# Performance work log

Hardware: AMD Instinct MI355X
Metric: run time of the kernel (lower is better)

The kernel has to match this reference:

```python
import jax, jax.numpy as jnp
import numpy as np

IS_CAUSAL = True
NEG_INF = float('-inf')


def setup_inputs() -> dict:
    key = jax.random.key(0)
    kq, kk, kv = jax.random.split(key, 3)
    B, H, S, D = 4, 16, 2048, 64
    return {
        'query': jax.random.normal(kq, (B, H, S, D), dtype=jnp.float32),
        'key': jax.random.normal(kk, (B, H, S, D), dtype=jnp.float32),
        'value': jax.random.normal(kv, (B, H, S, D), dtype=jnp.float32),
    }


def reference(query, key, value):
    # Attention(Q,K,V) = softmax(QK^T / sqrt(d_k) + causal_mask) V
    d_k = query.shape[-1]
    scale = 1.0 / np.sqrt(d_k).astype(np.float32)
    # [B,H,Sq,Sk]
    scores = jnp.einsum('bhqd,bhkd->bhqk', query, key) * scale
    if IS_CAUSAL:
        sq, sk = query.shape[-2], key.shape[-2]
        causal = jnp.triu(jnp.ones((sq, sk), dtype=bool), k=1)
        scores = jnp.where(causal[None, None, :, :], NEG_INF, scores)
    weights = jax.nn.softmax(scores, axis=-1)
    # dropout p=0.0 (eval): identity
    out = jnp.einsum('bhqk,bhkd->bhqd', weights, value)
    return out
```

## Files before the change

### kernel.cpp

```cpp
#include <hip/hip_runtime.h>
#include <stdint.h>


#define SLEN 2048
#define DHEAD 64
#define NHEADS 64
#define NELEM (SLEN * DHEAD * NHEADS)
#define PADP 72

typedef short bf16x8 __attribute__((ext_vector_type(8)));
typedef float f32x4 __attribute__((ext_vector_type(4)));

__device__ __forceinline__ uint32_t pkbf(float hi, float lo) {
    uint32_t a = __builtin_bit_cast(uint32_t, lo) + 0x8000u;
    uint32_t b = __builtin_bit_cast(uint32_t, hi) + 0x8000u;
    return __builtin_amdgcn_perm(b, a, 0x07060302u);
}
__device__ __forceinline__ unsigned short f2bf(float f) {
    return (unsigned short)((__builtin_bit_cast(uint32_t, f) + 0x8000u) >> 16);
}
__device__ __forceinline__ int swz(int row, int g) {
    return row * 64 + ((g ^ (row & 7)) << 3);
}

__global__ __launch_bounds__(256)
void convert_prep(const float* __restrict__ K, const float* __restrict__ V,
                  unsigned short* __restrict__ Kb, unsigned short* __restrict__ Vtb) {
    __shared__ unsigned short Lt[64 * 264];
    const int b = blockIdx.x, t = threadIdx.x;
    if (b < 4096) {
        const int off = (b * 256 + t) * 8;
        float4 a = *(const float4*)(K + off);
        float4 c = *(const float4*)(K + off + 4);
        uint4 o;
        o.x = pkbf(a.y, a.x); o.y = pkbf(a.w, a.z);
        o.z = pkbf(c.y, c.x); o.w = pkbf(c.w, c.z);
        *(uint4*)(Kb + off) = o;
    } else {
        const int vb2 = b - 4096;
        const int head = vb2 >> 3, kblk = vb2 & 7;
        const float* Vh = V + (size_t)head * (SLEN * DHEAD) + kblk * 256 * DHEAD;
        unsigned short* Vo = Vtb + (size_t)head * (SLEN * DHEAD) + kblk * 256;
#pragma unroll
        for (int i = 0; i < 16; ++i) {
            int idx = t + 256 * i;
            int key = idx >> 4, d4 = idx & 15;
            float4 v = *(const float4*)(Vh + key * DHEAD + d4 * 4);
            Lt[(d4 * 4 + 0) * 264 + key] = f2bf(v.x);
            Lt[(d4 * 4 + 1) * 264 + key] = f2bf(v.y);
            Lt[(d4 * 4 + 2) * 264 + key] = f2bf(v.z);
            Lt[(d4 * 4 + 3) * 264 + key] = f2bf(v.w);
        }
        __syncthreads();
#pragma unroll
        for (int j = 0; j < 8; ++j) {
            int idx = t + 256 * j;
            int d = idx >> 5, k8 = idx & 31;
            *(uint4*)(Vo + (size_t)d * SLEN + k8 * 8) = *(const uint4*)(Lt + d * 264 + k8 * 8);
        }
    }
}

__global__ __launch_bounds__(512, 4)
void sdpa_mfma(const float* __restrict__ Qf, const unsigned short* __restrict__ Kb,
               const unsigned short* __restrict__ Vtb, float* __restrict__ Og) {
    const int n    = blockIdx.x;
    const int half = n >> 8, idx = n & 255;
    const int head = idx >> 2, r4 = idx & 3;
    const int qb   = (half == 0) ? (4 + r4) : (3 - r4);
    const int q0   = qb * 256;

    const size_t hb = (size_t)head * SLEN * DHEAD;
    const float* Qh = Qf + hb;
    const unsigned short* Kh  = Kb + hb;
    const unsigned short* Vth = Vtb + hb;
    float* Oh = Og + hb;

    const int tid  = threadIdx.x;
    const int w    = tid >> 6, lane = tid & 63;
    const int cl   = lane & 15, quad = lane >> 4;

    __shared__ unsigned short Kl[64 * 64];
    __shared__ unsigned short Vt[64 * 64];
    __shared__ unsigned short Pl[8 * 32 * PADP];

    const int qw = q0 + w * 32;
    unsigned short* Plw = Pl + w * 32 * PADP;

    bf16x8 qf[2][2];
#pragma unroll
    for (int m = 0; m < 2; ++m)
#pragma unroll
        for (int h = 0; h < 2; ++h) {
            const float* src = Qh + (size_t)(qw + m * 16 + cl) * DHEAD + h * 32 + quad * 8;
            float4 a = *(const float4*)src;
            float4 c = *(const float4*)(src + 4);
            uint4 u;
            u.x = pkbf(a.y, a.x); u.y = pkbf(a.w, a.z);
            u.z = pkbf(c.y, c.x); u.w = pkbf(c.w, c.z);
            qf[m][h] = __builtin_bit_cast(bf16x8, u);
        }

    f32x4 o[2][4];
#pragma unroll
    for (int m = 0; m < 2; ++m)
#pragma unroll
        for (int d = 0; d < 4; ++d) o[m][d] = (f32x4){0.f, 0.f, 0.f, 0.f};
    float ls[2] = {0.f, 0.f};
    const float SCL = 0.18033688f;

    const int srow = tid >> 3, sg = tid & 7;
    const int ldsOff = swz(srow, sg);
    const size_t kSrc = (size_t)srow * DHEAD + sg * 8;
    const size_t vSrc = (size_t)srow * SLEN + sg * 8;

    const int ntiles = (qb + 1) * 4;
    uint4 kreg = *(const uint4*)(Kh + kSrc);
    uint4 vreg = *(const uint4*)(Vth + vSrc);

    for (int t = 0; t < ntiles; ++t) {
        const int k0 = t * 64;
        __syncthreads();
        *(uint4*)(Kl + ldsOff) = kreg;
        *(uint4*)(Vt + ldsOff) = vreg;
        __syncthreads();
        if (t + 1 < ntiles) {
            kreg = *(const uint4*)(Kh + kSrc + (size_t)(k0 + 64) * DHEAD);
            vreg = *(const uint4*)(Vth + vSrc + (k0 + 64));
        }
        if (k0 > qw + 31) continue;
        const bool partial = (k0 + 63 > qw);

        bf16x8 kb[4][2];
#pragma unroll
        for (int kk = 0; kk < 4; ++kk)
#pragma unroll
            for (int h = 0; h < 2; ++h)
                kb[kk][h] = __builtin_bit_cast(bf16x8,
                    *(const uint4*)(Kl + swz(kk * 16 + cl, h * 4 + quad)));

#pragma unroll
        for (int qq = 0; qq < 2; ++qq) {
            const int qrel = qw - k0 + qq * 16 + cl;
#pragma unroll
            for (int kk = 0; kk < 4; ++kk) {
                f32x4 s = (f32x4){0.f, 0.f, 0.f, 0.f};
                s = __builtin_amdgcn_mfma_f32_16x16x32_bf16(kb[kk][0], qf[qq][0], s, 0, 0, 0);
                s = __builtin_amdgcn_mfma_f32_16x16x32_bf16(kb[kk][1], qf[qq][1], s, 0, 0, 0);
                const int krel = kk * 16 + quad * 4;
                float p0, p1, p2, p3;
                if (partial) {
                    p0 = (krel + 0 <= qrel) ? __builtin_amdgcn_exp2f(s[0] * SCL) : 0.f;
                    p1 = (krel + 1 <= qrel) ? __builtin_amdgcn_exp2f(s[1] * SCL) : 0.f;
                    p2 = (krel + 2 <= qrel) ? __builtin_amdgcn_exp2f(s[2] * SCL) : 0.f;
                    p3 = (krel + 3 <= qrel) ? __builtin_amdgcn_exp2f(s[3] * SCL) : 0.f;
                } else {
                    p0 = __builtin_amdgcn_exp2f(s[0] * SCL);
                    p1 = __builtin_amdgcn_exp2f(s[1] * SCL);
                    p2 = __builtin_amdgcn_exp2f(s[2] * SCL);
                    p3 = __builtin_amdgcn_exp2f(s[3] * SCL);
                }
                ls[qq] += (p0 + p1) + (p2 + p3);
                uint2 pw;
                pw.x = pkbf(p1, p0);
                pw.y = pkbf(p3, p2);
                *(uint2*)(Plw + (qq * 16 + cl) * PADP + kk * 16 + quad * 4) = pw;
            }
        }

        bf16x8 pa[2][2], vbf[4][2];
#pragma unroll
        for (int m = 0; m < 2; ++m)
#pragma unroll
            for (int h = 0; h < 2; ++h)
                pa[m][h] = __builtin_bit_cast(bf16x8,
                    *(const uint4*)(Plw + (m * 16 + cl) * PADP + h * 32 + quad * 8));
#pragma unroll
        for (int dd = 0; dd < 4; ++dd)
#pragma unroll
            for (int h = 0; h < 2; ++h)
                vbf[dd][h] = __builtin_bit_cast(bf16x8,
                    *(const uint4*)(Vt + swz(dd * 16 + cl, h * 4 + quad)));

#pragma unroll
        for (int m = 0; m < 2; ++m)
#pragma unroll
            for (int dd = 0; dd < 4; ++dd) {
                o[m][dd] = __builtin_amdgcn_mfma_f32_16x16x32_bf16(pa[m][0], vbf[dd][0], o[m][dd], 0, 0, 0);
                o[m][dd] = __builtin_amdgcn_mfma_f32_16x16x32_bf16(pa[m][1], vbf[dd][1], o[m][dd], 0, 0, 0);
            }
    }

#pragma unroll
    for (int qq = 0; qq < 2; ++qq) {
        float v = ls[qq];
        v += __shfl_xor(v, 16);
        v += __shfl_xor(v, 32);
        ls[qq] = v;
    }

#pragma unroll
    for (int m = 0; m < 2; ++m)
#pragma unroll
        for (int r = 0; r < 4; ++r) {
            const float inv = 1.0f / __shfl(ls[m], quad * 4 + r);
#pragma unroll
            for (int dd = 0; dd < 4; ++dd)
                Oh[(size_t)(qw + m * 16 + quad * 4 + r) * DHEAD + dd * 16 + cl] = o[m][dd][r] * inv;
        }
}

extern "C" void kernel_launch(void* const* d_in, const int* in_sizes, int n_in,
                              void* d_out, int out_size, void* d_ws, size_t ws_size,
                              hipStream_t stream) {
    const float* Q = (const float*)d_in[0];
    const float* K = (const float*)d_in[1];
    const float* V = (const float*)d_in[2];
    float*       O = (float*)d_out;

    unsigned short* Kbf  = (unsigned short*)d_ws;
    unsigned short* Vtbf = Kbf + NELEM;

    convert_prep<<<dim3(4096 + 512), dim3(256), 0, stream>>>(K, V, Kbf, Vtbf);
    sdpa_mfma<<<dim3(512), dim3(512), 0, stream>>>(Q, Kbf, Vtbf, O);
}
```

Measured before the change: 219.5 us.

## Pair complementary 64-row query blocks per workgroup and shrink blocks to 256 threads

Each workgroup now has 4 waves covering two 64-row query blocks, A and 31-A. Their causal tile counts sum to a constant, so work per workgroup is balanced, and the grid doubles to 1024 blocks. Each thread loads two K/V vectors per tile. The K and V fragment loads are also interleaved with the MFMAs to cut register pressure. The cost is that waves owning block A sit idle during the later tiles that only block 31-A needs, while staying through the barriers.

```diff
diff --git a/kernel.cpp b/kernel.cpp
--- a/kernel.cpp
+++ b/kernel.cpp
@@ -53,22 +53,22 @@
         }
         __syncthreads();
 #pragma unroll
-        for (int j = 0; j < 8; ++j) {
-            int idx = t + 256 * j;
+        for (int jj = 0; jj < 8; ++jj) {
+            int idx = t + 256 * jj;
             int d = idx >> 5, k8 = idx & 31;
             *(uint4*)(Vo + (size_t)d * SLEN + k8 * 8) = *(const uint4*)(Lt + d * 264 + k8 * 8);
         }
     }
 }
 
-__global__ __launch_bounds__(512, 4)
+__global__ __launch_bounds__(256, 4)
 void sdpa_mfma(const float* __restrict__ Qf, const unsigned short* __restrict__ Kb,
                const unsigned short* __restrict__ Vtb, float* __restrict__ Og) {
-    const int n    = blockIdx.x;
-    const int half = n >> 8, idx = n & 255;
-    const int head = idx >> 2, r4 = idx & 3;
-    const int qb   = (half == 0) ? (4 + r4) : (3 - r4);
-    const int q0   = qb * 256;
+    const int n = blockIdx.x;
+    const int j = n >> 8, c = n & 255;
+    const int head = c & 63;
+    const int A  = (c >> 6) + 4 * j;
+    const int Bq = 31 - A;
 
     const size_t hb = (size_t)head * SLEN * DHEAD;
     const float* Qh = Qf + hb;
@@ -82,9 +82,9 @@
 
     __shared__ unsigned short Kl[64 * 64];
     __shared__ unsigned short Vt[64 * 64];
-    __shared__ unsigned short Pl[8 * 32 * PADP];
-
-    const int qw = q0 + w * 32;
+    __shared__ unsigned short Pl[4 * 32 * PADP];
+
+    const int qw = ((w < 2) ? A * 64 : Bq * 64) + (w & 1) * 32;
     unsigned short* Plw = Pl + w * 32 * PADP;
 
     bf16x8 qf[2][2];
@@ -94,10 +94,10 @@
         for (int h = 0; h < 2; ++h) {
             const float* src = Qh + (size_t)(qw + m * 16 + cl) * DHEAD + h * 32 + quad * 8;
             float4 a = *(const float4*)src;
-            float4 c = *(const float4*)(src + 4);
+            float4 b = *(const float4*)(src + 4);
             uint4 u;
             u.x = pkbf(a.y, a.x); u.y = pkbf(a.w, a.z);
-            u.z = pkbf(c.y, c.x); u.w = pkbf(c.w, c.z);
+            u.z = pkbf(b.y, b.x); u.w = pkbf(b.w, b.z);
             qf[m][h] = __builtin_bit_cast(bf16x8, u);
         }
 
@@ -109,66 +109,65 @@
     float ls[2] = {0.f, 0.f};
     const float SCL = 0.18033688f;
 
-    const int srow = tid >> 3, sg = tid & 7;
-    const int ldsOff = swz(srow, sg);
-    const size_t kSrc = (size_t)srow * DHEAD + sg * 8;
-    const size_t vSrc = (size_t)srow * SLEN + sg * 8;
-
-    const int ntiles = (qb + 1) * 4;
-    uint4 kreg = *(const uint4*)(Kh + kSrc);
-    uint4 vreg = *(const uint4*)(Vth + vSrc);
+    const int p1 = tid + 256;
+    const int srow0 = tid >> 3, sg0 = tid & 7;
+    const int srow1 = p1 >> 3,  sg1 = p1 & 7;
+    const int lo0 = swz(srow0, sg0), lo1 = swz(srow1, sg1);
+    const size_t kS0 = (size_t)srow0 * DHEAD + sg0 * 8, kS1 = (size_t)srow1 * DHEAD + sg1 * 8;
+    const size_t vS0 = (size_t)srow0 * SLEN + sg0 * 8,  vS1 = (size_t)srow1 * SLEN + sg1 * 8;
+
+    const int ntiles = Bq + 1;
+    uint4 kr0 = *(const uint4*)(Kh + kS0), kr1 = *(const uint4*)(Kh + kS1);
+    uint4 vr0 = *(const uint4*)(Vth + vS0), vr1 = *(const uint4*)(Vth + vS1);
 
     for (int t = 0; t < ntiles; ++t) {
         const int k0 = t * 64;
         __syncthreads();
-        *(uint4*)(Kl + ldsOff) = kreg;
-        *(uint4*)(Vt + ldsOff) = vreg;
+        *(uint4*)(Kl + lo0) = kr0; *(uint4*)(Kl + lo1) = kr1;
+        *(uint4*)(Vt + lo0) = vr0; *(uint4*)(Vt + lo1) = vr1;
         __syncthreads();
         if (t + 1 < ntiles) {
-            kreg = *(const uint4*)(Kh + kSrc + (size_t)(k0 + 64) * DHEAD);
-            vreg = *(const uint4*)(Vth + vSrc + (k0 + 64));
+            const size_t ko = (size_t)(k0 + 64) * DHEAD;
+            kr0 = *(const uint4*)(Kh + kS0 + ko);
+            kr1 = *(const uint4*)(Kh + kS1 + ko);
+            vr0 = *(const uint4*)(Vth + vS0 + (k0 + 64));
+            vr1 = *(const uint4*)(Vth + vS1 + (k0 + 64));
         }
         if (k0 > qw + 31) continue;
         const bool partial = (k0 + 63 > qw);
 
-        bf16x8 kb[4][2];
-#pragma unroll
-        for (int kk = 0; kk < 4; ++kk)
-#pragma unroll
-            for (int h = 0; h < 2; ++h)
-                kb[kk][h] = __builtin_bit_cast(bf16x8,
-                    *(const uint4*)(Kl + swz(kk * 16 + cl, h * 4 + quad)));
-
-#pragma unroll
-        for (int qq = 0; qq < 2; ++qq) {
-            const int qrel = qw - k0 + qq * 16 + cl;
-#pragma unroll
-            for (int kk = 0; kk < 4; ++kk) {
+#pragma unroll
+        for (int kk = 0; kk < 4; ++kk) {
+            bf16x8 kb0 = __builtin_bit_cast(bf16x8, *(const uint4*)(Kl + swz(kk * 16 + cl, quad)));
+            bf16x8 kb1 = __builtin_bit_cast(bf16x8, *(const uint4*)(Kl + swz(kk * 16 + cl, 4 + quad)));
+            const int krel = kk * 16 + quad * 4;
+#pragma unroll
+            for (int qq = 0; qq < 2; ++qq) {
                 f32x4 s = (f32x4){0.f, 0.f, 0.f, 0.f};
-                s = __builtin_amdgcn_mfma_f32_16x16x32_bf16(kb[kk][0], qf[qq][0], s, 0, 0, 0);
-                s = __builtin_amdgcn_mfma_f32_16x16x32_bf16(kb[kk][1], qf[qq][1], s, 0, 0, 0);
-                const int krel = kk * 16 + quad * 4;
-                float p0, p1, p2, p3;
+                s = __builtin_amdgcn_mfma_f32_16x16x32_bf16(kb0, qf[qq][0], s, 0, 0, 0);
+                s = __builtin_amdgcn_mfma_f32_16x16x32_bf16(kb1, qf[qq][1], s, 0, 0, 0);
+                float p0, p1v, p2, p3;
                 if (partial) {
+                    const int qrel = qw - k0 + qq * 16 + cl;
                     p0 = (krel + 0 <= qrel) ? __builtin_amdgcn_exp2f(s[0] * SCL) : 0.f;
-                    p1 = (krel + 1 <= qrel) ? __builtin_amdgcn_exp2f(s[1] * SCL) : 0.f;
+                    p1v = (krel + 1 <= qrel) ? __builtin_amdgcn_exp2f(s[1] * SCL) : 0.f;
                     p2 = (krel + 2 <= qrel) ? __builtin_amdgcn_exp2f(s[2] * SCL) : 0.f;
                     p3 = (krel + 3 <= qrel) ? __builtin_amdgcn_exp2f(s[3] * SCL) : 0.f;
                 } else {
                     p0 = __builtin_amdgcn_exp2f(s[0] * SCL);
-                    p1 = __builtin_amdgcn_exp2f(s[1] * SCL);
+                    p1v = __builtin_amdgcn_exp2f(s[1] * SCL);
                     p2 = __builtin_amdgcn_exp2f(s[2] * SCL);
                     p3 = __builtin_amdgcn_exp2f(s[3] * SCL);
                 }
-                ls[qq] += (p0 + p1) + (p2 + p3);
+                ls[qq] += (p0 + p1v) + (p2 + p3);
                 uint2 pw;
-                pw.x = pkbf(p1, p0);
+                pw.x = pkbf(p1v, p0);
                 pw.y = pkbf(p3, p2);
                 *(uint2*)(Plw + (qq * 16 + cl) * PADP + kk * 16 + quad * 4) = pw;
             }
         }
 
-        bf16x8 pa[2][2], vbf[4][2];
+        bf16x8 pa[2][2];
 #pragma unroll
         for (int m = 0; m < 2; ++m)
 #pragma unroll
@@ -176,19 +175,15 @@
                 pa[m][h] = __builtin_bit_cast(bf16x8,
                     *(const uint4*)(Plw + (m * 16 + cl) * PADP + h * 32 + quad * 8));
 #pragma unroll
-        for (int dd = 0; dd < 4; ++dd)
-#pragma unroll
-            for (int h = 0; h < 2; ++h)
-                vbf[dd][h] = __builtin_bit_cast(bf16x8,
-                    *(const uint4*)(Vt + swz(dd * 16 + cl, h * 4 + quad)));
-
-#pragma unroll
-        for (int m = 0; m < 2; ++m)
-#pragma unroll
-            for (int dd = 0; dd < 4; ++dd) {
-                o[m][dd] = __builtin_amdgcn_mfma_f32_16x16x32_bf16(pa[m][0], vbf[dd][0], o[m][dd], 0, 0, 0);
-                o[m][dd] = __builtin_amdgcn_mfma_f32_16x16x32_bf16(pa[m][1], vbf[dd][1], o[m][dd], 0, 0, 0);
+        for (int dd = 0; dd < 4; ++dd) {
+            bf16x8 vb0 = __builtin_bit_cast(bf16x8, *(const uint4*)(Vt + swz(dd * 16 + cl, quad)));
+            bf16x8 vb1 = __builtin_bit_cast(bf16x8, *(const uint4*)(Vt + swz(dd * 16 + cl, 4 + quad)));
+#pragma unroll
+            for (int m = 0; m < 2; ++m) {
+                o[m][dd] = __builtin_amdgcn_mfma_f32_16x16x32_bf16(pa[m][0], vb0, o[m][dd], 0, 0, 0);
+                o[m][dd] = __builtin_amdgcn_mfma_f32_16x16x32_bf16(pa[m][1], vb1, o[m][dd], 0, 0, 0);
             }
+        }
     }
 
 #pragma unroll
@@ -222,5 +217,5 @@
     unsigned short* Vtbf = Kbf + NELEM;
 
     convert_prep<<<dim3(4096 + 512), dim3(256), 0, stream>>>(K, V, Kbf, Vtbf);
-    sdpa_mfma<<<dim3(512), dim3(512), 0, stream>>>(Q, Kbf, Vtbf, O);
-}
+    sdpa_mfma<<<dim3(1024), dim3(256), 0, stream>>>(Q, Kbf, Vtbf, O);
+}
```

Measured after the change: 196.5 us. 1.12x faster.

## Rebalance causal attention into paired 64-row tiles with split-K across two waves

Applied to the files above, without the earlier changes.

Replaces the 512-thread blocks that stage K/V tiles in shared memory with 128-thread blocks (two waves). Each block handles a short query tile A and its mirrored long tile 31-A, splitting the long tile's key range between the waves and merging partial outputs and row sums through LDS. K and V fragments are now loaded straight from global/L2 with one-step register prefetch of K, and the softmax scale is folded into Q. This aims to balance causal work per block and drop the per-tile block-wide barriers, at the cost of redundant global reads of K/V per wave and far fewer threads per block.

```diff
diff --git a/kernel.cpp b/kernel.cpp
--- a/kernel.cpp
+++ b/kernel.cpp
@@ -7,6 +7,7 @@
 #define NHEADS 64
 #define NELEM (SLEN * DHEAD * NHEADS)
 #define PADP 72
+#define OMPAD 68
 
 typedef short bf16x8 __attribute__((ext_vector_type(8)));
 typedef float f32x4 __attribute__((ext_vector_type(4)));
@@ -18,9 +19,6 @@
 }
 __device__ __forceinline__ unsigned short f2bf(float f) {
     return (unsigned short)((__builtin_bit_cast(uint32_t, f) + 0x8000u) >> 16);
-}
-__device__ __forceinline__ int swz(int row, int g) {
-    return row * 64 + ((g ^ (row & 7)) << 3);
 }
 
 __global__ __launch_bounds__(256)
@@ -53,22 +51,21 @@
         }
         __syncthreads();
 #pragma unroll
-        for (int j = 0; j < 8; ++j) {
-            int idx = t + 256 * j;
+        for (int jj = 0; jj < 8; ++jj) {
+            int idx = t + 256 * jj;
             int d = idx >> 5, k8 = idx & 31;
             *(uint4*)(Vo + (size_t)d * SLEN + k8 * 8) = *(const uint4*)(Lt + d * 264 + k8 * 8);
         }
     }
 }
 
-__global__ __launch_bounds__(512, 4)
+__global__ __launch_bounds__(128, 2)
 void sdpa_mfma(const float* __restrict__ Qf, const unsigned short* __restrict__ Kb,
                const unsigned short* __restrict__ Vtb, float* __restrict__ Og) {
     const int n    = blockIdx.x;
-    const int half = n >> 8, idx = n & 255;
-    const int head = idx >> 2, r4 = idx & 3;
-    const int qb   = (half == 0) ? (4 + r4) : (3 - r4);
-    const int q0   = qb * 256;
+    const int head = n & 63;
+    const int A    = n >> 6;
+    const int TB   = 31 - A;
 
     const size_t hb = (size_t)head * SLEN * DHEAD;
     const float* Qh = Qf + hb;
@@ -80,134 +77,172 @@
     const int w    = tid >> 6, lane = tid & 63;
     const int cl   = lane & 15, quad = lane >> 4;
 
-    __shared__ unsigned short Kl[64 * 64];
-    __shared__ unsigned short Vt[64 * 64];
-    __shared__ unsigned short Pl[8 * 32 * PADP];
-
-    const int qw = q0 + w * 32;
-    unsigned short* Plw = Pl + w * 32 * PADP;
-
-    bf16x8 qf[2][2];
-#pragma unroll
-    for (int m = 0; m < 2; ++m)
-#pragma unroll
-        for (int h = 0; h < 2; ++h) {
-            const float* src = Qh + (size_t)(qw + m * 16 + cl) * DHEAD + h * 32 + quad * 8;
-            float4 a = *(const float4*)src;
-            float4 c = *(const float4*)(src + 4);
-            uint4 u;
-            u.x = pkbf(a.y, a.x); u.y = pkbf(a.w, a.z);
-            u.z = pkbf(c.y, c.x); u.w = pkbf(c.w, c.z);
-            qf[m][h] = __builtin_bit_cast(bf16x8, u);
-        }
-
-    f32x4 o[2][4];
-#pragma unroll
-    for (int m = 0; m < 2; ++m)
-#pragma unroll
-        for (int d = 0; d < 4; ++d) o[m][d] = (f32x4){0.f, 0.f, 0.f, 0.f};
-    float ls[2] = {0.f, 0.f};
+    __shared__ unsigned short Pl[2 * 64 * PADP];
+    __shared__ float Om[64 * OMPAD];
+    __shared__ float Lsm[64];
+
+    unsigned short* Plw = Pl + w * 64 * PADP;
     const float SCL = 0.18033688f;
 
-    const int srow = tid >> 3, sg = tid & 7;
-    const int ldsOff = swz(srow, sg);
-    const size_t kSrc = (size_t)srow * DHEAD + sg * 8;
-    const size_t vSrc = (size_t)srow * SLEN + sg * 8;
-
-    const int ntiles = (qb + 1) * 4;
-    uint4 kreg = *(const uint4*)(Kh + kSrc);
-    uint4 vreg = *(const uint4*)(Vth + vSrc);
-
-    for (int t = 0; t < ntiles; ++t) {
-        const int k0 = t * 64;
-        __syncthreads();
-        *(uint4*)(Kl + ldsOff) = kreg;
-        *(uint4*)(Vt + ldsOff) = vreg;
-        __syncthreads();
-        if (t + 1 < ntiles) {
-            kreg = *(const uint4*)(Kh + kSrc + (size_t)(k0 + 64) * DHEAD);
-            vreg = *(const uint4*)(Vth + vSrc + (k0 + 64));
-        }
-        if (k0 > qw + 31) continue;
-        const bool partial = (k0 + 63 > qw);
-
-        bf16x8 kb[4][2];
+    bf16x8 qf[4][2];
+    bf16x8 kbn[4][2];
+    f32x4  o[4][4];
+    float  ls[4];
+
+    auto load_qf = [&](int qw) {
+#pragma unroll
+        for (int m = 0; m < 4; ++m)
+#pragma unroll
+            for (int h = 0; h < 2; ++h) {
+                const float* src = Qh + (size_t)(qw + m * 16 + cl) * DHEAD + h * 32 + quad * 8;
+                float4 a = *(const float4*)src;
+                float4 b = *(const float4*)(src + 4);
+                uint4 u;
+                u.x = pkbf(a.y * SCL, a.x * SCL); u.y = pkbf(a.w * SCL, a.z * SCL);
+                u.z = pkbf(b.y * SCL, b.x * SCL); u.w = pkbf(b.w * SCL, b.z * SCL);
+                qf[m][h] = __builtin_bit_cast(bf16x8, u);
+            }
+    };
+    auto zero_acc = [&]() {
+#pragma unroll
+        for (int m = 0; m < 4; ++m) {
+            ls[m] = 0.f;
+#pragma unroll
+            for (int d = 0; d < 4; ++d) o[m][d] = (f32x4){0.f, 0.f, 0.f, 0.f};
+        }
+    };
+    auto load_kb = [&](int j, bf16x8 kb[4][2]) {
+        const unsigned short* base = Kh + (size_t)j * 64 * DHEAD;
 #pragma unroll
         for (int kk = 0; kk < 4; ++kk)
 #pragma unroll
             for (int h = 0; h < 2; ++h)
                 kb[kk][h] = __builtin_bit_cast(bf16x8,
-                    *(const uint4*)(Kl + swz(kk * 16 + cl, h * 4 + quad)));
-
-#pragma unroll
-        for (int qq = 0; qq < 2; ++qq) {
-            const int qrel = qw - k0 + qq * 16 + cl;
+                    *(const uint4*)(base + (kk * 16 + cl) * DHEAD + h * 32 + quad * 8));
+    };
+
+    auto do_steps = [&](int tq, int js, int je) {
+        if (js >= je) return;
+        load_kb(js, kbn);
+        for (int j = js; j < je; ++j) {
+            bf16x8 vb[4][2];
+            const unsigned short* vbase = Vth + j * 64;
+#pragma unroll
+            for (int dd = 0; dd < 4; ++dd)
+#pragma unroll
+                for (int h = 0; h < 2; ++h)
+                    vb[dd][h] = __builtin_bit_cast(bf16x8,
+                        *(const uint4*)(vbase + (size_t)(dd * 16 + cl) * SLEN + h * 32 + quad * 8));
+
+            const bool partial = (j == tq);
 #pragma unroll
             for (int kk = 0; kk < 4; ++kk) {
-                f32x4 s = (f32x4){0.f, 0.f, 0.f, 0.f};
-                s = __builtin_amdgcn_mfma_f32_16x16x32_bf16(kb[kk][0], qf[qq][0], s, 0, 0, 0);
-                s = __builtin_amdgcn_mfma_f32_16x16x32_bf16(kb[kk][1], qf[qq][1], s, 0, 0, 0);
                 const int krel = kk * 16 + quad * 4;
-                float p0, p1, p2, p3;
-                if (partial) {
-                    p0 = (krel + 0 <= qrel) ? __builtin_amdgcn_exp2f(s[0] * SCL) : 0.f;
-                    p1 = (krel + 1 <= qrel) ? __builtin_amdgcn_exp2f(s[1] * SCL) : 0.f;
-                    p2 = (krel + 2 <= qrel) ? __builtin_amdgcn_exp2f(s[2] * SCL) : 0.f;
-                    p3 = (krel + 3 <= qrel) ? __builtin_amdgcn_exp2f(s[3] * SCL) : 0.f;
-                } else {
-                    p0 = __builtin_amdgcn_exp2f(s[0] * SCL);
-                    p1 = __builtin_amdgcn_exp2f(s[1] * SCL);
-                    p2 = __builtin_amdgcn_exp2f(s[2] * SCL);
-                    p3 = __builtin_amdgcn_exp2f(s[3] * SCL);
+#pragma unroll
+                for (int qq = 0; qq < 4; ++qq) {
+                    f32x4 s = (f32x4){0.f, 0.f, 0.f, 0.f};
+                    s = __builtin_amdgcn_mfma_f32_16x16x32_bf16(kbn[kk][0], qf[qq][0], s, 0, 0, 0);
+                    s = __builtin_amdgcn_mfma_f32_16x16x32_bf16(kbn[kk][1], qf[qq][1], s, 0, 0, 0);
+                    float p0, p1, p2, p3;
+                    if (partial) {
+                        const int qrel = qq * 16 + cl;
+                        p0 = (krel + 0 <= qrel) ? __builtin_amdgcn_exp2f(s[0]) : 0.f;
+                        p1 = (krel + 1 <= qrel) ? __builtin_amdgcn_exp2f(s[1]) : 0.f;
+                        p2 = (krel + 2 <= qrel) ? __builtin_amdgcn_exp2f(s[2]) : 0.f;
+                        p3 = (krel + 3 <= qrel) ? __builtin_amdgcn_exp2f(s[3]) : 0.f;
+                    } else {
+                        p0 = __builtin_amdgcn_exp2f(s[0]);
+                        p1 = __builtin_amdgcn_exp2f(s[1]);
+                        p2 = __builtin_amdgcn_exp2f(s[2]);
+                        p3 = __builtin_amdgcn_exp2f(s[3]);
+                    }
+                    ls[qq] += (p0 + p1) + (p2 + p3);
+                    uint2 pw;
+                    pw.x = pkbf(p1, p0);
+                    pw.y = pkbf(p3, p2);
+                    *(uint2*)(Plw + (qq * 16 + cl) * PADP + kk * 16 + quad * 4) = pw;
                 }
-                ls[qq] += (p0 + p1) + (p2 + p3);
-                uint2 pw;
-                pw.x = pkbf(p1, p0);
-                pw.y = pkbf(p3, p2);
-                *(uint2*)(Plw + (qq * 16 + cl) * PADP + kk * 16 + quad * 4) = pw;
             }
-        }
-
-        bf16x8 pa[2][2], vbf[4][2];
-#pragma unroll
-        for (int m = 0; m < 2; ++m)
-#pragma unroll
-            for (int h = 0; h < 2; ++h)
-                pa[m][h] = __builtin_bit_cast(bf16x8,
-                    *(const uint4*)(Plw + (m * 16 + cl) * PADP + h * 32 + quad * 8));
-#pragma unroll
-        for (int dd = 0; dd < 4; ++dd)
-#pragma unroll
-            for (int h = 0; h < 2; ++h)
-                vbf[dd][h] = __builtin_bit_cast(bf16x8,
-                    *(const uint4*)(Vt + swz(dd * 16 + cl, h * 4 + quad)));
-
-#pragma unroll
-        for (int m = 0; m < 2; ++m)
-#pragma unroll
-            for (int dd = 0; dd < 4; ++dd) {
-                o[m][dd] = __builtin_amdgcn_mfma_f32_16x16x32_bf16(pa[m][0], vbf[dd][0], o[m][dd], 0, 0, 0);
-                o[m][dd] = __builtin_amdgcn_mfma_f32_16x16x32_bf16(pa[m][1], vbf[dd][1], o[m][dd], 0, 0, 0);
+            const int jn = (j + 1 < je) ? j + 1 : j;
+            load_kb(jn, kbn);
+
+            bf16x8 pa[4][2];
+#pragma unroll
+            for (int m = 0; m < 4; ++m)
+#pragma unroll
+                for (int h = 0; h < 2; ++h)
+                    pa[m][h] = __builtin_bit_cast(bf16x8,
+                        *(const uint4*)(Plw + (m * 16 + cl) * PADP + h * 32 + quad * 8));
+#pragma unroll
+            for (int m = 0; m < 4; ++m)
+#pragma unroll
+                for (int dd = 0; dd < 4; ++dd) {
+                    o[m][dd] = __builtin_amdgcn_mfma_f32_16x16x32_bf16(pa[m][0], vb[dd][0], o[m][dd], 0, 0, 0);
+                    o[m][dd] = __builtin_amdgcn_mfma_f32_16x16x32_bf16(pa[m][1], vb[dd][1], o[m][dd], 0, 0, 0);
+                }
+        }
+    };
+    auto reduce_ls = [&]() {
+#pragma unroll
+        for (int qq = 0; qq < 4; ++qq) {
+            float v = ls[qq];
+            v += __shfl_xor(v, 16);
+            v += __shfl_xor(v, 32);
+            ls[qq] = v;
+        }
+    };
+    auto store_tile = [&](int qw, const float lsr[4]) {
+#pragma unroll
+        for (int m = 0; m < 4; ++m)
+#pragma unroll
+            for (int r = 0; r < 4; ++r) {
+                const float inv = 1.0f / __shfl(lsr[m], quad * 4 + r);
+#pragma unroll
+                for (int dd = 0; dd < 4; ++dd)
+                    Oh[(size_t)(qw + m * 16 + quad * 4 + r) * DHEAD + dd * 16 + cl] = o[m][dd][r] * inv;
             }
-    }
-
-#pragma unroll
-    for (int qq = 0; qq < 2; ++qq) {
-        float v = ls[qq];
-        v += __shfl_xor(v, 16);
-        v += __shfl_xor(v, 32);
-        ls[qq] = v;
-    }
-
-#pragma unroll
-    for (int m = 0; m < 2; ++m)
-#pragma unroll
-        for (int r = 0; r < 4; ++r) {
-            const float inv = 1.0f / __shfl(ls[m], quad * 4 + r);
+    };
+
+    if (w == 0) {
+        load_qf(A * 64);
+        zero_acc();
+        do_steps(A, 0, A + 1);
+        reduce_ls();
+        store_tile(A * 64, ls);
+        load_qf(TB * 64);
+        zero_acc();
+        do_steps(TB, 0, 16 - A);
+        reduce_ls();
+    } else {
+        load_qf(TB * 64);
+        zero_acc();
+        do_steps(TB, 16 - A, 32 - A);
+        reduce_ls();
+    }
+
+    if (w == 1) {
+#pragma unroll
+        for (int m = 0; m < 4; ++m)
 #pragma unroll
             for (int dd = 0; dd < 4; ++dd)
-                Oh[(size_t)(qw + m * 16 + quad * 4 + r) * DHEAD + dd * 16 + cl] = o[m][dd][r] * inv;
-        }
+                *(f32x4*)(Om + (dd * 16 + cl) * OMPAD + m * 16 + quad * 4) = o[m][dd];
+        if (quad == 0) {
+#pragma unroll
+            for (int qq = 0; qq < 4; ++qq) Lsm[qq * 16 + cl] = ls[qq];
+        }
+    }
+    __syncthreads();
+    if (w == 0) {
+#pragma unroll
+        for (int m = 0; m < 4; ++m)
+#pragma unroll
+            for (int dd = 0; dd < 4; ++dd)
+                o[m][dd] += *(const f32x4*)(Om + (dd * 16 + cl) * OMPAD + m * 16 + quad * 4);
+        float lc[4];
+#pragma unroll
+        for (int qq = 0; qq < 4; ++qq) lc[qq] = ls[qq] + Lsm[qq * 16 + cl];
+        store_tile(TB * 64, lc);
+    }
 }
 
 extern "C" void kernel_launch(void* const* d_in, const int* in_sizes, int n_in,
@@ -222,5 +257,5 @@
     unsigned short* Vtbf = Kbf + NELEM;
 
     convert_prep<<<dim3(4096 + 512), dim3(256), 0, stream>>>(K, V, Kbf, Vtbf);
-    sdpa_mfma<<<dim3(512), dim3(512), 0, stream>>>(Q, Kbf, Vtbf, O);
-}
+    sdpa_mfma<<<dim3(1024), dim3(128), 0, stream>>>(Q, Kbf, Vtbf, O);
+}
```

New measurement: 205.2 us. 6.5% less time.
